# Performance work log

Hardware: AMD Instinct MI355X
Metric: run time of the kernel (lower is better)

Reference implementation:

```python
import jax, jax.numpy as jnp
import numpy as np

K = 4
G = 64
IN_DIM = 256
OUT_DIM = 256
BATCH = 512
T0, T1 = -1.0, 1.0


def setup_inputs() -> dict:
    key = jax.random.key(0)
    kx, kw = jax.random.split(key)
    x = jax.random.uniform(kx, (BATCH, IN_DIM), jnp.float32, T0, T1)
    # xavier_normal_ on [G+K, in, out]: std = sqrt(2 / (fan_in + fan_out)) with fan over last two dims
    std = (2.0 / (IN_DIM + OUT_DIM)) ** 0.5
    w = jax.random.normal(kw, (G + K, IN_DIM, OUT_DIM), jnp.float32) * std
    # knot vector: k-1 repeats of t0, linspace(t0,t1,G+1), k-1 repeats of t1
    t = jnp.concatenate([
        jnp.full((K - 1,), T0, jnp.float32),
        jnp.linspace(T0, T1, G + 1, dtype=jnp.float32),
        jnp.full((K - 1,), T1, jnp.float32),
    ])
    return {"x": x, "w": w, "t": t, "k": K}


def _basis(x, t, k):
    """Cox-de Boor: the k nonzero order-k B-spline basis values at each x.
    Returns (idx, N): idx [..., k] basis indices i-k+1..i, N [..., k] values."""
    n_t = t.shape[0]
    # interval i with t[i] <= x < t[i+1], clipped to the valid span
    i = jnp.clip(jnp.searchsorted(t, x, side='right') - 1, k - 1, n_t - k - 1)
    N = jnp.ones(x.shape + (1,), x.dtype)
    for p in range(1, k):  # static small loop (k=4)
        jj = jnp.arange(1, p + 1)
        left = x[..., None] - t[i[..., None] + 1 - jj]   # [..., p]
        right = t[i[..., None] + jj] - x[..., None]      # [..., p]
        saved = jnp.zeros_like(x)
        vals = []
        for r in range(p):
            d = right[..., r] + left[..., p - 1 - r]      # t[i+r+1] - t[i+r+1-p]
            temp = N[..., r] / d
            vals.append(saved + right[..., r] * temp)
            saved = left[..., p - 1 - r] * temp
        vals.append(saved)
        N = jnp.stack(vals, -1)
    idx = i[..., None] - (k - 1) + jnp.arange(k)
    return idx, N


def reference(x, w, t, k):
    in_dim = x.shape[1]
    n_rows = w.shape[0]
    idx, y1 = _basis(x, t, k)                             # [B,in,k], [B,in,k]
    # last row of w (index -1 == n_rows-1) weights the SiLU residual term
    idx_full = jnp.concatenate(
        [idx, jnp.full(idx.shape[:-1] + (1,), n_rows - 1, idx.dtype)], -1)  # [B,in,k+1]
    silu = x * jax.nn.sigmoid(x)
    y2 = jnp.concatenate([y1, silu[..., None]], -1)       # [B,in,k+1]
    # gather local spline coefficients: w2[b,c,j,o] = w[idx_full[b,c,j], c, o]
    w2 = w[idx_full, jnp.arange(in_dim)[None, :, None], :]  # [B,in,k+1,out]
    return jnp.einsum('bcjo,bcj->bo', w2, y2)             # [B,out]
```

## Files before the change

### kernel.cpp

```cpp
#include <hip/hip_runtime.h>
#include <math.h>
#include <stdint.h>

#define IN_DIM  256
#define OUT_DIM 256
#define NROWS   68
#define NT      71
#define BATCH   512
#define W_ELEMS (NROWS * IN_DIM * OUT_DIM)
#define PART_FLOATS (8 * BATCH * OUT_DIM)

__device__ __forceinline__ uint32_t bf16_rne(float f) {
  uint32_t u = __builtin_bit_cast(uint32_t, f);
  return (u + 0x7fffu + ((u >> 16) & 1u)) >> 16;
}

__global__ __launch_bounds__(256) void cvt_kernel(const float* __restrict__ w,
                                                  uint32_t* __restrict__ wb) {
  const int base = (blockIdx.x * 256 + threadIdx.x) * 8;
  const float4 a = *(const float4*)(w + base);
  const float4 b = *(const float4*)(w + base + 4);
  uint4 o;
  o.x = bf16_rne(a.x) | (bf16_rne(a.y) << 16);
  o.y = bf16_rne(a.z) | (bf16_rne(a.w) << 16);
  o.z = bf16_rne(b.x) | (bf16_rne(b.y) << 16);
  o.w = bf16_rne(b.z) | (bf16_rne(b.w) << 16);
  *(uint4*)(wb + base / 2) = o;
}

__device__ __forceinline__ void fma8(const uint4 q, const float y, float* acc) {
  acc[0] += y * __builtin_bit_cast(float, q.x << 16);
  acc[1] += y * __builtin_bit_cast(float, q.x & 0xffff0000u);
  acc[2] += y * __builtin_bit_cast(float, q.y << 16);
  acc[3] += y * __builtin_bit_cast(float, q.y & 0xffff0000u);
  acc[4] += y * __builtin_bit_cast(float, q.z << 16);
  acc[5] += y * __builtin_bit_cast(float, q.z & 0xffff0000u);
  acc[6] += y * __builtin_bit_cast(float, q.w << 16);
  acc[7] += y * __builtin_bit_cast(float, q.w & 0xffff0000u);
}

__global__ __launch_bounds__(256) void kan_gather_kernel(
    const float* __restrict__ x, const uint4* __restrict__ wp,
    const float* __restrict__ t, float* __restrict__ part) {
  __shared__ float  lt[NT];
  __shared__ float4 nA[32][8];
  __shared__ float  sA[32][8];
  __shared__ int    bA[32][8];
  __shared__ float  red[4][2048];

  const int tid = threadIdx.x;
  const unsigned bid = blockIdx.x;
  const int cchunk = bid & 7;
  const int bgroup = bid >> 3;

  if (tid < NT) lt[tid] = t[tid];
  __syncthreads();

  {
    const int bb = tid >> 5;
    const int cl = tid & 31;
    const float xv = x[(size_t)(bgroup * 8 + bb) * IN_DIM + cchunk * 32 + cl];
    int i = 3 + (int)floorf((xv + 1.0f) * 32.0f);
    i = i < 3 ? 3 : (i > 66 ? 66 : i);
    while (i > 3 && xv < lt[i]) --i;
    while (i < 66 && xv >= lt[i + 1]) ++i;

    float N0 = 1.f, N1 = 0.f, N2 = 0.f, N3 = 0.f;
    {
      const float l1 = xv - lt[i];
      const float r1 = lt[i + 1] - xv;
      const float tp = N0 / (r1 + l1);
      N1 = l1 * tp; N0 = r1 * tp;
    }
    {
      const float l1 = xv - lt[i];
      const float l2 = xv - lt[i - 1];
      const float r1 = lt[i + 1] - xv;
      const float r2 = lt[i + 2] - xv;
      float saved = 0.f;
      const float tp0 = N0 / (r1 + l2);
      const float n0 = saved + r1 * tp0; saved = l2 * tp0;
      const float tp1 = N1 / (r2 + l1);
      const float n1 = saved + r2 * tp1; saved = l1 * tp1;
      N0 = n0; N1 = n1; N2 = saved;
    }
    {
      const float l1 = xv - lt[i];
      const float l2 = xv - lt[i - 1];
      const float l3 = xv - lt[i - 2];
      const float r1 = lt[i + 1] - xv;
      const float r2 = lt[i + 2] - xv;
      const float r3 = lt[i + 3] - xv;
      float saved = 0.f;
      const float tp0 = N0 / (r1 + l3);
      const float n0 = saved + r1 * tp0; saved = l3 * tp0;
      const float tp1 = N1 / (r2 + l2);
      const float n1 = saved + r2 * tp1; saved = l2 * tp1;
      const float tp2 = N2 / (r3 + l1);
      const float n2 = saved + r3 * tp2; saved = l1 * tp2;
      N0 = n0; N1 = n1; N2 = n2; N3 = saved;
    }
    nA[cl][bb] = make_float4(N0, N1, N2, N3);
    sA[cl][bb] = xv / (1.0f + expf(-xv));
    bA[cl][bb] = i - 3;
  }
  __syncthreads();

  const int wv   = tid >> 6;
  const int lane = tid & 63;
  const int half = lane >> 5;
  const int ol   = lane & 31;

  float acc[8][8];
  #pragma unroll
  for (int b = 0; b < 8; ++b) {
    #pragma unroll
    for (int j = 0; j < 8; ++j) acc[b][j] = 0.f;
  }

  for (int pp = 0; pp < 4; ++pp) {
    const int cl = wv * 8 + pp * 2 + half;
    const uint32_t cbase = (uint32_t)((cchunk * 32 + cl) * 32 + ol);
    const uint4 q4 = wp[cbase + 67u * 8192u];

    uint4 q[8][4];
    #pragma unroll
    for (int b = 0; b < 8; ++b) {
      const uint32_t rb = cbase + ((uint32_t)bA[cl][b] << 13);
      q[b][0] = wp[rb];
      q[b][1] = wp[rb +  8192u];
      q[b][2] = wp[rb + 16384u];
      q[b][3] = wp[rb + 24576u];
    }
    #pragma unroll
    for (int b = 0; b < 8; ++b) {
      const float4 yv = nA[cl][b];
      const float  ys = sA[cl][b];
      fma8(q[b][0], yv.x, acc[b]);
      fma8(q[b][1], yv.y, acc[b]);
      fma8(q[b][2], yv.z, acc[b]);
      fma8(q[b][3], yv.w, acc[b]);
      fma8(q4,      ys,   acc[b]);
    }
  }

  #pragma unroll
  for (int b = 0; b < 8; ++b) {
    #pragma unroll
    for (int j = 0; j < 8; ++j)
      acc[b][j] += __shfl_xor(acc[b][j], 32, 64);
  }

  if (half == 0) {
    #pragma unroll
    for (int b = 0; b < 8; ++b) {
      #pragma unroll
      for (int j = 0; j < 8; ++j)
        red[wv][b * 256 + ol * 8 + j] = acc[b][j];
    }
  }
  __syncthreads();

  {
    const int b  = tid >> 5;
    const int oo = tid & 31;
    float s[8] = {0.f, 0.f, 0.f, 0.f, 0.f, 0.f, 0.f, 0.f};
    #pragma unroll
    for (int w2 = 0; w2 < 4; ++w2) {
      const float* rr = &red[w2][b * 256 + oo * 8];
      #pragma unroll
      for (int j = 0; j < 8; ++j) s[j] += rr[j];
    }
    float* dst = part + ((size_t)cchunk * BATCH + bgroup * 8 + b) * OUT_DIM + oo * 8;
    *(float4*)dst       = make_float4(s[0], s[1], s[2], s[3]);
    *(float4*)(dst + 4) = make_float4(s[4], s[5], s[6], s[7]);
  }
}

__global__ __launch_bounds__(256) void reduce_kernel(const float* __restrict__ part,
                                                     float* __restrict__ out) {
  const int q = blockIdx.x * 256 + threadIdx.x;
  const int S = BATCH * OUT_DIM / 4;
  const float4* p = (const float4*)part;
  float4 s = p[q];
  #pragma unroll
  for (int k = 1; k < 8; ++k) {
    const float4 a = p[q + k * S];
    s.x += a.x; s.y += a.y; s.z += a.z; s.w += a.w;
  }
  ((float4*)out)[q] = s;
}

extern "C" void kernel_launch(void* const* d_in, const int* in_sizes, int n_in,
                              void* d_out, int out_size, void* d_ws, size_t ws_size,
                              hipStream_t stream) {
  const float* x = (const float*)d_in[0];
  const float* w = (const float*)d_in[1];
  const float* t = (const float*)d_in[2];
  float* out  = (float*)d_out;
  float* part = (float*)d_ws;
  uint32_t* wb = (uint32_t*)d_ws + PART_FLOATS;
  cvt_kernel<<<W_ELEMS / (256 * 8), 256, 0, stream>>>(w, wb);
  kan_gather_kernel<<<BATCH / 8 * 8, 256, 0, stream>>>(x, (const uint4*)wb, t, part);
  reduce_kernel<<<BATCH * OUT_DIM / 4 / 256, 256, 0, stream>>>(part, out);
}
```

Baseline: 89.88 us.

## Assign gather work items per XCD via atomic queues for L2 locality

Each block reads its hardware XCD id and claims a work item from a per-XCD atomic counter, so all batch groups for one input-channel chunk run on the same XCD and share its L2 cache for that chunk's weight slices. If an XCD's queue is exhausted, the block steals from the others. The counters are zeroed inside the conversion kernel. This adds an atomic and a shared-memory broadcast at block start, and it relies on a reading of the XCD id hardware register.

```diff
diff --git a/kernel.cpp b/kernel.cpp
--- a/kernel.cpp
+++ b/kernel.cpp
@@ -9,6 +9,7 @@
 #define BATCH   512
 #define W_ELEMS (NROWS * IN_DIM * OUT_DIM)
 #define PART_FLOATS (8 * BATCH * OUT_DIM)
+#define WB_U32S (W_ELEMS / 2)
 
 __device__ __forceinline__ uint32_t bf16_rne(float f) {
   uint32_t u = __builtin_bit_cast(uint32_t, f);
@@ -16,7 +17,9 @@
 }
 
 __global__ __launch_bounds__(256) void cvt_kernel(const float* __restrict__ w,
-                                                  uint32_t* __restrict__ wb) {
+                                                  uint32_t* __restrict__ wb,
+                                                  int* __restrict__ qcnt) {
+  if (blockIdx.x == 0 && threadIdx.x < 8) qcnt[threadIdx.x] = 0;
   const int base = (blockIdx.x * 256 + threadIdx.x) * 8;
   const float4 a = *(const float4*)(w + base);
   const float4 b = *(const float4*)(w + base + 4);
@@ -41,20 +44,34 @@
 
 __global__ __launch_bounds__(256) void kan_gather_kernel(
     const float* __restrict__ x, const uint4* __restrict__ wp,
-    const float* __restrict__ t, float* __restrict__ part) {
+    const float* __restrict__ t, float* __restrict__ part,
+    int* __restrict__ qcnt) {
   __shared__ float  lt[NT];
   __shared__ float4 nA[32][8];
   __shared__ float  sA[32][8];
   __shared__ int    bA[32][8];
   __shared__ float  red[4][2048];
+  __shared__ int    s_item;
 
   const int tid = threadIdx.x;
-  const unsigned bid = blockIdx.x;
-  const int cchunk = bid & 7;
-  const int bgroup = bid >> 3;
-
+
+  if (tid == 0) {
+    uint32_t xcd;
+    asm volatile("s_getreg_b32 %0, hwreg(20, 0, 4)" : "=s"(xcd));
+    int item = -1;
+    #pragma unroll 1
+    for (int d = 0; d < 8 && item < 0; ++d) {
+      const int qx = (int)((xcd + d) & 7);
+      const int n = atomicAdd(&qcnt[qx], 1);
+      if (n < 64) item = qx * 64 + n;
+    }
+    s_item = item;
+  }
   if (tid < NT) lt[tid] = t[tid];
   __syncthreads();
+
+  const int cchunk = s_item >> 6;
+  const int bgroup = s_item & 63;
 
   {
     const int bb = tid >> 5;
@@ -200,7 +217,8 @@
   float* out  = (float*)d_out;
   float* part = (float*)d_ws;
   uint32_t* wb = (uint32_t*)d_ws + PART_FLOATS;
-  cvt_kernel<<<W_ELEMS / (256 * 8), 256, 0, stream>>>(w, wb);
-  kan_gather_kernel<<<BATCH / 8 * 8, 256, 0, stream>>>(x, (const uint4*)wb, t, part);
+  int* qcnt = (int*)(wb + WB_U32S);
+  cvt_kernel<<<W_ELEMS / (256 * 8), 256, 0, stream>>>(w, wb, qcnt);
+  kan_gather_kernel<<<512, 256, 0, stream>>>(x, (const uint4*)wb, t, part, qcnt);
   reduce_kernel<<<BATCH * OUT_DIM / 4 / 256, 256, 0, stream>>>(part, out);
 }
```

Measured after the change: 94.83 us. 5.5% more time.

## Fuse split-K reduction into gather kernel via atomic counters; switch weights to fp16

Applied to the files above, without the earlier changes.

Removes the separate reduce kernel. Each batch group keeps an atomic counter, and the last of its 8 channel-chunk blocks sums the partials and writes the output, which saves one launch and a full pass over the partials. The flags are zeroed inside the conversion kernel. The weight compression also changes from bf16 to fp16 with hardware conversion, giving more mantissa precision at similar cost.

```diff
diff --git a/kernel.cpp b/kernel.cpp
--- a/kernel.cpp
+++ b/kernel.cpp
@@ -1,4 +1,5 @@
 #include <hip/hip_runtime.h>
+#include <hip/hip_fp16.h>
 #include <math.h>
 #include <stdint.h>
 
@@ -9,44 +10,52 @@
 #define BATCH   512
 #define W_ELEMS (NROWS * IN_DIM * OUT_DIM)
 #define PART_FLOATS (8 * BATCH * OUT_DIM)
-
-__device__ __forceinline__ uint32_t bf16_rne(float f) {
-  uint32_t u = __builtin_bit_cast(uint32_t, f);
-  return (u + 0x7fffu + ((u >> 16) & 1u)) >> 16;
-}
+#define WB_U32S (W_ELEMS / 2)
 
 __global__ __launch_bounds__(256) void cvt_kernel(const float* __restrict__ w,
-                                                  uint32_t* __restrict__ wb) {
+                                                  uint32_t* __restrict__ wb,
+                                                  int* __restrict__ flags) {
+  if (blockIdx.x == 0 && threadIdx.x < 64) flags[threadIdx.x] = 0;
   const int base = (blockIdx.x * 256 + threadIdx.x) * 8;
   const float4 a = *(const float4*)(w + base);
   const float4 b = *(const float4*)(w + base + 4);
   uint4 o;
-  o.x = bf16_rne(a.x) | (bf16_rne(a.y) << 16);
-  o.y = bf16_rne(a.z) | (bf16_rne(a.w) << 16);
-  o.z = bf16_rne(b.x) | (bf16_rne(b.y) << 16);
-  o.w = bf16_rne(b.z) | (bf16_rne(b.w) << 16);
+  o.x = (uint32_t)__half_as_ushort(__float2half_rn(a.x)) |
+        ((uint32_t)__half_as_ushort(__float2half_rn(a.y)) << 16);
+  o.y = (uint32_t)__half_as_ushort(__float2half_rn(a.z)) |
+        ((uint32_t)__half_as_ushort(__float2half_rn(a.w)) << 16);
+  o.z = (uint32_t)__half_as_ushort(__float2half_rn(b.x)) |
+        ((uint32_t)__half_as_ushort(__float2half_rn(b.y)) << 16);
+  o.w = (uint32_t)__half_as_ushort(__float2half_rn(b.z)) |
+        ((uint32_t)__half_as_ushort(__float2half_rn(b.w)) << 16);
   *(uint4*)(wb + base / 2) = o;
 }
 
 __device__ __forceinline__ void fma8(const uint4 q, const float y, float* acc) {
-  acc[0] += y * __builtin_bit_cast(float, q.x << 16);
-  acc[1] += y * __builtin_bit_cast(float, q.x & 0xffff0000u);
-  acc[2] += y * __builtin_bit_cast(float, q.y << 16);
-  acc[3] += y * __builtin_bit_cast(float, q.y & 0xffff0000u);
-  acc[4] += y * __builtin_bit_cast(float, q.z << 16);
-  acc[5] += y * __builtin_bit_cast(float, q.z & 0xffff0000u);
-  acc[6] += y * __builtin_bit_cast(float, q.w << 16);
-  acc[7] += y * __builtin_bit_cast(float, q.w & 0xffff0000u);
+  const __half2 h0 = __builtin_bit_cast(__half2, q.x);
+  const __half2 h1 = __builtin_bit_cast(__half2, q.y);
+  const __half2 h2 = __builtin_bit_cast(__half2, q.z);
+  const __half2 h3 = __builtin_bit_cast(__half2, q.w);
+  acc[0] += y * __half2float(h0.x);
+  acc[1] += y * __half2float(h0.y);
+  acc[2] += y * __half2float(h1.x);
+  acc[3] += y * __half2float(h1.y);
+  acc[4] += y * __half2float(h2.x);
+  acc[5] += y * __half2float(h2.y);
+  acc[6] += y * __half2float(h3.x);
+  acc[7] += y * __half2float(h3.y);
 }
 
 __global__ __launch_bounds__(256) void kan_gather_kernel(
     const float* __restrict__ x, const uint4* __restrict__ wp,
-    const float* __restrict__ t, float* __restrict__ part) {
+    const float* __restrict__ t, float* __restrict__ part,
+    int* __restrict__ flags, float* __restrict__ out) {
   __shared__ float  lt[NT];
   __shared__ float4 nA[32][8];
   __shared__ float  sA[32][8];
   __shared__ int    bA[32][8];
   __shared__ float  red[4][2048];
+  __shared__ int    s_old;
 
   const int tid = threadIdx.x;
   const unsigned bid = blockIdx.x;
@@ -161,9 +170,9 @@
   }
   __syncthreads();
 
+  const int b  = tid >> 5;
+  const int oo = tid & 31;
   {
-    const int b  = tid >> 5;
-    const int oo = tid & 31;
     float s[8] = {0.f, 0.f, 0.f, 0.f, 0.f, 0.f, 0.f, 0.f};
     #pragma unroll
     for (int w2 = 0; w2 < 4; ++w2) {
@@ -175,20 +184,34 @@
     *(float4*)dst       = make_float4(s[0], s[1], s[2], s[3]);
     *(float4*)(dst + 4) = make_float4(s[4], s[5], s[6], s[7]);
   }
-}
-
-__global__ __launch_bounds__(256) void reduce_kernel(const float* __restrict__ part,
-                                                     float* __restrict__ out) {
-  const int q = blockIdx.x * 256 + threadIdx.x;
-  const int S = BATCH * OUT_DIM / 4;
-  const float4* p = (const float4*)part;
-  float4 s = p[q];
-  #pragma unroll
-  for (int k = 1; k < 8; ++k) {
-    const float4 a = p[q + k * S];
-    s.x += a.x; s.y += a.y; s.z += a.z; s.w += a.w;
-  }
-  ((float4*)out)[q] = s;
+
+  __syncthreads();
+  if (tid == 0) {
+    __threadfence();
+    s_old = atomicAdd(&flags[bgroup], 1);
+  }
+  __syncthreads();
+  if (s_old == 7) {
+    if (tid == 0) __threadfence();
+    __syncthreads();
+    const float* pb = part + ((size_t)bgroup * 8 + b) * OUT_DIM + oo * 8;
+    const int S = BATCH * OUT_DIM;
+    float4 lo[8], hi[8];
+    #pragma unroll
+    for (int k = 0; k < 8; ++k) {
+      lo[k] = *(const float4*)(pb + (size_t)k * S);
+      hi[k] = *(const float4*)(pb + (size_t)k * S + 4);
+    }
+    float4 s0 = lo[0], s1 = hi[0];
+    #pragma unroll
+    for (int k = 1; k < 8; ++k) {
+      s0.x += lo[k].x; s0.y += lo[k].y; s0.z += lo[k].z; s0.w += lo[k].w;
+      s1.x += hi[k].x; s1.y += hi[k].y; s1.z += hi[k].z; s1.w += hi[k].w;
+    }
+    float* d = out + ((size_t)bgroup * 8 + b) * OUT_DIM + oo * 8;
+    *(float4*)d       = s0;
+    *(float4*)(d + 4) = s1;
+  }
 }
 
 extern "C" void kernel_launch(void* const* d_in, const int* in_sizes, int n_in,
@@ -200,7 +223,7 @@
   float* out  = (float*)d_out;
   float* part = (float*)d_ws;
   uint32_t* wb = (uint32_t*)d_ws + PART_FLOATS;
-  cvt_kernel<<<W_ELEMS / (256 * 8), 256, 0, stream>>>(w, wb);
-  kan_gather_kernel<<<BATCH / 8 * 8, 256, 0, stream>>>(x, (const uint4*)wb, t, part);
-  reduce_kernel<<<BATCH * OUT_DIM / 4 / 256, 256, 0, stream>>>(part, out);
-}
+  int* flags = (int*)(wb + WB_U32S);
+  cvt_kernel<<<W_ELEMS / (256 * 8), 256, 0, stream>>>(w, wb, flags);
+  kan_gather_kernel<<<512, 256, 0, stream>>>(x, (const uint4*)wb, t, part, flags, out);
+}
```

Result: slower. 116.6 us (+29.7%).
